# Optimization experiments

Hardware: AMD Instinct MI355X
Metric: run time of the kernel (lower is better)

Reference implementation:

```python
import jax, jax.numpy as jnp
import numpy as np

L_IN, L_ENC, B = 1024, 1024, 16
D_IN, D_ENC, D_EMB = 512, 512, 512


def setup_inputs() -> dict:
    key = jax.random.key(0)
    ks = jax.random.split(key, 9)
    s_in = 1.0 / np.sqrt(D_IN)
    s_emb = 1.0 / np.sqrt(D_EMB)
    s_enc = 1.0 / np.sqrt(D_ENC)
    return {
        "in_seq": jax.random.normal(ks[0], (L_IN, B, D_IN), jnp.float32),
        "enc_seq": jax.random.normal(ks[1], (L_ENC, B, D_ENC), jnp.float32),
        "prev_target_seq": jax.random.normal(ks[2], (L_IN, B, D_EMB), jnp.float32),
        # torch Linear weights: (out_features, in_features)
        "W_in2enc": jax.random.normal(ks[3], (D_ENC, D_IN), jnp.float32) * s_in,
        "b_in2enc": jnp.zeros((D_ENC,), jnp.float32),
        "W_lab2enc": jax.random.normal(ks[4], (D_ENC, D_EMB), jnp.float32) * s_emb,
        "b_lab2enc": jnp.zeros((D_ENC,), jnp.float32),
        "W_enc2in": jax.random.normal(ks[5], (D_IN, D_ENC), jnp.float32) * s_enc,
        "b_enc2in": jnp.zeros((D_IN,), jnp.float32),
    }


def reference(in_seq, enc_seq, prev_target_seq,
              W_in2enc, b_in2enc, W_lab2enc, b_lab2enc, W_enc2in, b_enc2in):
    # d_vals: (L_in, B, D_enc) = proj(in_seq) + proj(prev_target_seq)
    in_proj = jnp.einsum('lbi,ei->lbe', in_seq, W_in2enc) + b_in2enc
    tgt_proj = jnp.einsum('lbm,em->lbe', prev_target_seq, W_lab2enc) + b_lab2enc
    d_vals = in_proj + tgt_proj
    # raw attention scores: (L_in, L_enc, B) dot products over D_enc
    scores = jnp.einsum('lbe,mbe->lmb', d_vals, enc_seq)
    # sum-normalization (NOT softmax) over the encoder-length axis
    attn = scores / jnp.sum(scores, axis=1, keepdims=True)
    # weighted sum of encoder states: (L_in, B, D_enc)
    context = jnp.einsum('lmb,mbe->lbe', attn, enc_seq)
    # project back to input dim
    return jnp.einsum('lbe,ie->lbi', context, W_enc2in) + b_enc2in
```

## Files before the change

kernel.cpp:

```cpp
#include <hip/hip_runtime.h>
#include <cstdint>

static constexpr int LDR = 8192;

typedef uint16_t u16;
typedef __attribute__((ext_vector_type(8))) short short8;
typedef __attribute__((ext_vector_type(4))) float f32x4;
struct alignas(8) U16x4 { u16 x, y, z, w; };

__device__ __forceinline__ u16 f2bf(float f) {
    union { float f; unsigned u; } v; v.f = f;
    unsigned r = v.u + 0x7fffu + ((v.u >> 16) & 1u);
    return (u16)(r >> 16);
}

__device__ __forceinline__ short8 cvt8(const float4 a, const float4 b) {
    short8 r;
    r[0]=(short)f2bf(a.x); r[1]=(short)f2bf(a.y); r[2]=(short)f2bf(a.z); r[3]=(short)f2bf(a.w);
    r[4]=(short)f2bf(b.x); r[5]=(short)f2bf(b.y); r[6]=(short)f2bf(b.z); r[7]=(short)f2bf(b.w);
    return r;
}

__device__ __forceinline__ void gl_lds16(const u16* g, unsigned ldsaddr) {
    asm volatile("s_mov_b32 m0, %0\n\t"
                 "global_load_lds_dwordx4 %1, off"
                 :: "s"(__builtin_amdgcn_readfirstlane(ldsaddr)), "v"(g)
                 : "memory");
}

template<int MODE>
__device__ __forceinline__ void gemm_body(
    int bx, int by, int z,
    const u16* __restrict__ A, const u16* __restrict__ Bm,
    const float* __restrict__ b1v, const float* __restrict__ b2v,
    const float* __restrict__ b3v, const float* __restrict__ Sinv,
    u16* __restrict__ Cb, float* __restrict__ Cf)
{
    constexpr int K   = (MODE == 1 || MODE == 5) ? 1024 : 512;
    constexpr int BM  = (MODE == 5 || MODE == 6) ? 64 : 128;
    constexpr int NJ  = (BM == 128) ? 4 : 2;
    constexpr int NIA = BM / 64;
    constexpr int NIB = 2;
    constexpr int ASZ = BM * 64;
    constexpr int BSZ = 128 * 64;
    constexpr int LDA = (MODE == 1 || MODE == 5) ? 1024 : 512;
    constexpr int LDB = (MODE == 1 || MODE == 5) ? 1024 : 512;
    constexpr bool PRIO = (MODE == 5 || MODE == 6);

    extern __shared__ __align__(16) u16 lds[];

    const int row0 = by * BM;
    const int col0 = bx * 128;
    const int tid  = threadIdx.x;
    const int l    = tid & 63, w = tid >> 6;
    const int wm   = (BM == 128) ? (w >> 1) : 0;
    const int wn   = (BM == 128) ? (w & 1) : w;
    const int quad = l >> 4, l16 = l & 15;

    const u16* Ab = A;
    const u16* Bb = Bm;
    if constexpr (MODE == 5) { Ab = A + z*524288; Bb = Bm + z*524288; }
    if constexpr (MODE == 6) { Bb = Bm + z*262144; }
    if constexpr (MODE == 4) { Ab = A + z*524288; Bb = Bm + z*262144; }

    const int lr = l >> 2;
    const int loffu = ((l & 3) ^ (lr & 3)) * 8;
    const u16* gA[NIA];
    #pragma unroll
    for (int i = 0; i < NIA; ++i)
        gA[i] = Ab + (size_t)(row0 + i*64 + w*16 + lr) * LDA + loffu;
    const u16* gB[NIB];
    #pragma unroll
    for (int i = 0; i < NIB; ++i)
        gB[i] = Bb + (size_t)(col0 + i*64 + w*16 + lr) * LDB + loffu;

    const unsigned lbase = (unsigned)(size_t)&lds[0];

    auto stage = [&](int c) {
        #pragma unroll
        for (int i = 0; i < NIA; ++i) {
            gl_lds16(gA[i], lbase + c*ASZ + i*4096 + w*1024);
            gA[i] += 32;
        }
        #pragma unroll
        for (int i = 0; i < NIB; ++i) {
            gl_lds16(gB[i], lbase + 2*ASZ + c*BSZ + i*4096 + w*1024);
            gB[i] += 32;
        }
    };

    f32x4 acc[4][NJ] = {};
    const int swzr = (l16 & 3) << 3;
    const int arow = wm * 64;
    const int brow = wn * (BM == 128 ? 64 : 32);
    const int koff = (quad * 8) ^ swzr;

    stage(0);
    int cur = 0;
    for (int kb = 0; kb < K; kb += 32) {
        asm volatile("s_waitcnt vmcnt(0)" ::: "memory");
        __syncthreads();
        if (kb + 32 < K) stage(cur ^ 1);
        const int abase = cur * (ASZ/2);
        const int bbase = ASZ + cur * (BSZ/2);
        short8 af[4], bfr[NJ];
        #pragma unroll
        for (int i = 0; i < 4; ++i)
            af[i] = *(const short8*)&lds[abase + (arow + i*16 + l16)*32 + koff];
        #pragma unroll
        for (int j = 0; j < NJ; ++j)
            bfr[j] = *(const short8*)&lds[bbase + (brow + j*16 + l16)*32 + koff];
        if constexpr (PRIO) __builtin_amdgcn_s_setprio(1);
        #pragma unroll
        for (int i = 0; i < 4; ++i)
            #pragma unroll
            for (int j = 0; j < NJ; ++j)
                acc[i][j] = __builtin_amdgcn_mfma_f32_16x16x32_bf16(af[i], bfr[j], acc[i][j], 0, 0, 0);
        if constexpr (PRIO) __builtin_amdgcn_s_setprio(0);
        __syncthreads();
        cur ^= 1;
    }

    #pragma unroll
    for (int i = 0; i < 4; ++i) {
        const int grow = row0 + arow + i*16 + quad*4;
        #pragma unroll
        for (int j = 0; j < NJ; ++j) {
            const int gcol = col0 + brow + j*16 + l16;
            #pragma unroll
            for (int r = 0; r < 4; ++r) {
                float v = acc[i][j][r];
                const int R = grow + r;
                if constexpr (MODE == 1) {
                    v += b1v[gcol] + b2v[gcol];
                    Cb[((R & 15)*1024 + (R >> 4))*512 + gcol] = f2bf(v);
                } else if constexpr (MODE == 5 || MODE == 6) {
                    Cb[z*262144 + R*512 + gcol] = f2bf(v);
                } else {
                    const float s = Sinv[R*16 + z];
                    Cf[(R*16 + z)*512 + gcol] = v * s + b3v[gcol];
                }
            }
        }
    }
}

__device__ __forceinline__ void s_xt_body(
    int bid, const float* __restrict__ X, const float* __restrict__ T,
    const double* __restrict__ u, const double* __restrict__ cd,
    float* __restrict__ Sinv, u16* __restrict__ XT)
{
    const int wave = threadIdx.x >> 6, lane = threadIdx.x & 63;
    const int b = bid & 15, g = bid >> 4;
    const int e = lane * 8;
    double u1r[8], u2r[8];
    #pragma unroll
    for (int k = 0; k < 8; ++k) {
        u1r[k] = u[b*512 + e + k];
        u2r[k] = u[8192 + b*512 + e + k];
    }
    const double cb = cd[b];
    #pragma unroll 2
    for (int i = 0; i < 8; ++i) {
        const int j = g*32 + wave*8 + i;
        const int r = j*16 + b;
        float4 x0 = *(const float4*)&X[r*512 + e];
        float4 x1 = *(const float4*)&X[r*512 + e + 4];
        float4 t0 = *(const float4*)&T[r*512 + e];
        float4 t1 = *(const float4*)&T[r*512 + e + 4];
        double a = 0.0;
        a += (double)x0.x*u1r[0] + (double)x0.y*u1r[1] + (double)x0.z*u1r[2] + (double)x0.w*u1r[3];
        a += (double)x1.x*u1r[4] + (double)x1.y*u1r[5] + (double)x1.z*u1r[6] + (double)x1.w*u1r[7];
        a += (double)t0.x*u2r[0] + (double)t0.y*u2r[1] + (double)t0.z*u2r[2] + (double)t0.w*u2r[3];
        a += (double)t1.x*u2r[4] + (double)t1.y*u2r[5] + (double)t1.z*u2r[6] + (double)t1.w*u2r[7];
        *(short8*)&XT[r*1024 + e]       = cvt8(x0, x1);
        *(short8*)&XT[r*1024 + 512 + e] = cvt8(t0, t1);
        #pragma unroll
        for (int off = 32; off > 0; off >>= 1) a += __shfl_down(a, off, 64);
        if (lane == 0) Sinv[r] = (float)(1.0 / (a + cb));
    }
}

__global__ __launch_bounds__(256) void enct_wconv(
    const float* __restrict__ E, u16* __restrict__ EncT, double* __restrict__ part,
    const float* __restrict__ W1, const float* __restrict__ W2,
    const float* __restrict__ W3, u16* __restrict__ W12, u16* __restrict__ W3b)
{
    const int bid = blockIdx.x, t = threadIdx.x;
    if (bid >= 2048) {
        const int idx = (bid - 2048)*256 + t;
        if (idx < 65536) {
            const int r = idx >> 7, k8 = (idx & 127) * 8;
            const float* src = (k8 < 512) ? (W1 + r*512 + k8) : (W2 + r*512 + (k8 - 512));
            float4 a = *(const float4*)src;
            float4 b = *((const float4*)src + 1);
            *(short8*)&W12[r*1024 + k8] = cvt8(a, b);
        } else {
            const int i2 = idx - 65536;
            const int r = i2 >> 6, k8 = (i2 & 63) * 8;
            const float* src = W3 + r*512 + k8;
            float4 a = *(const float4*)src;
            float4 b = *((const float4*)src + 1);
            *(short8*)&W3b[r*512 + k8] = cvt8(a, b);
        }
        return;
    }
    __shared__ float tile[64][65];
    __shared__ double sred[256];
    const int ex = bid & 7;
    const int my = (bid >> 3) & 15;
    const int bb = bid >> 7;
    const int m0 = my * 64;
    const int e0 = ex * 64;
    const int tr = t >> 4;
    const int tc4 = (t & 15) * 4;
    #pragma unroll
    for (int it = 0; it < 4; ++it) {
        const int ml = tr + it*16;
        float4 v = *(const float4*)&E[(m0+ml)*LDR + bb*512 + e0 + tc4];
        *(float4*)&tile[ml][tc4] = v;
    }
    __syncthreads();
    #pragma unroll
    for (int it = 0; it < 4; ++it) {
        const int el = tr + it*16;
        U16x4 o;
        o.x = f2bf(tile[tc4+0][el]);
        o.y = f2bf(tile[tc4+1][el]);
        o.z = f2bf(tile[tc4+2][el]);
        o.w = f2bf(tile[tc4+3][el]);
        *(U16x4*)&EncT[bb*524288 + (e0+el)*1024 + m0 + tc4] = o;
    }
    const int el = t & 63, mq = t >> 6;
    double a = 0.0;
    #pragma unroll
    for (int j = 0; j < 16; ++j) a += (double)tile[mq*16 + j][el];
    sred[t] = a;
    __syncthreads();
    if (t < 64) {
        double s = sred[t] + sred[t+64] + sred[t+128] + sred[t+192];
        part[my*8192 + bb*512 + e0 + t] = s;
    }
}

__global__ __launch_bounds__(256) void g5_prep(
    const u16* __restrict__ EncT, u16* __restrict__ Gram,
    const float* __restrict__ W1, const float* __restrict__ W2,
    const float* __restrict__ b1, const float* __restrict__ b2,
    const double* __restrict__ part, double* __restrict__ u, double* __restrict__ cd)
{
    const int bid = blockIdx.x, tid = threadIdx.x;
    if (bid < 512) {
        gemm_body<5>(bid & 3, (bid >> 2) & 7, bid >> 5,
                     EncT, EncT, nullptr, nullptr, nullptr, nullptr, Gram, nullptr);
        return;
    }
    extern __shared__ __align__(16) u16 lds[];
    double* es_l = (double*)lds;
    double* red  = (double*)((char*)lds + 4096);
    const int blk = bid - 512;
    int b;
    if (blk < 64) b = (blk & 31) >> 1;
    else          b = blk - 64;
    for (int e = tid; e < 512; e += 256) {
        double s = 0.0;
        #pragma unroll
        for (int c = 0; c < 16; ++c) s += part[c*8192 + b*512 + e];
        es_l[e] = s;
    }
    __syncthreads();
    if (blk < 64) {
        const int which = blk >> 5;
        const int t = (blk & 31)*256 + tid;
        const int i = t & 511;
        const float* W = which ? W2 : W1;
        double a = 0.0;
        for (int e = 0; e < 512; ++e) a += (double)W[e*512 + i] * es_l[e];
        u[which*8192 + t] = a;
    } else {
        double a = 0.0;
        for (int e = tid; e < 512; e += 256) a += (double)(b1[e] + b2[e]) * es_l[e];
        red[tid] = a; __syncthreads();
        for (int s = 128; s > 0; s >>= 1) { if (tid < s) red[tid] += red[tid+s]; __syncthreads(); }
        if (tid == 0) cd[b] = red[0];
    }
}

__global__ __launch_bounds__(256) void g6_sxt(
    const u16* __restrict__ W3b, const u16* __restrict__ Gram, u16* __restrict__ HT,
    const float* __restrict__ X, const float* __restrict__ T,
    const double* __restrict__ u, const double* __restrict__ cd,
    float* __restrict__ Sinv, u16* __restrict__ XT)
{
    const int bid = blockIdx.x;
    const int idx = bid >> 1;
    if (bid & 1) {
        s_xt_body(idx, X, T, u, cd, Sinv, XT);
    } else {
        gemm_body<6>(idx & 3, (idx >> 2) & 7, idx >> 5,
                     W3b, Gram, nullptr, nullptr, nullptr, nullptr, HT, nullptr);
    }
}

__global__ __launch_bounds__(256) void gemm_m1(
    const u16* __restrict__ XT, const u16* __restrict__ W12,
    const float* __restrict__ b1, const float* __restrict__ b2,
    u16* __restrict__ dvals_g)
{
    const int bid = blockIdx.x;
    const int logical = (bid & 7)*64 + (bid >> 3);
    gemm_body<1>(logical & 3, logical >> 2, 0,
                 XT, W12, b1, b2, nullptr, nullptr, dvals_g, nullptr);
}

__global__ __launch_bounds__(256) void gemm_m4(
    const u16* __restrict__ dvals_g, const u16* __restrict__ HT,
    const float* __restrict__ b3, const float* __restrict__ Sinv,
    float* __restrict__ out)
{
    const int bid = blockIdx.x;
    const int logical = (bid & 7)*64 + (bid >> 3);
    gemm_body<4>(logical & 3, (logical >> 2) & 7, logical >> 5,
                 dvals_g, HT, nullptr, nullptr, b3, Sinv, nullptr, out);
}

extern "C" void kernel_launch(void* const* d_in, const int* in_sizes, int n_in,
                              void* d_out, int out_size, void* d_ws, size_t ws_size,
                              hipStream_t stream)
{
    const float* X   = (const float*)d_in[0];
    const float* Enc = (const float*)d_in[1];
    const float* T   = (const float*)d_in[2];
    const float* W1  = (const float*)d_in[3];
    const float* b1  = (const float*)d_in[4];
    const float* W2  = (const float*)d_in[5];
    const float* b2  = (const float*)d_in[6];
    const float* W3  = (const float*)d_in[7];
    const float* b3  = (const float*)d_in[8];
    float* out = (float*)d_out;

    char* w = (char*)d_ws;
    u16*    dvals_g  = (u16*)(w);
    u16*    EncT_bf  = (u16*)(w + 16777216);
    u16*    Gram_bf  = (u16*)(w + 33554432);
    u16*    HT_bf    = (u16*)(w + 41943040);
    u16*    W12      = (u16*)(w + 50331648);
    u16*    W3b      = (u16*)(w + 51380224);
    double* part     = (double*)(w + 51904512);
    double* u        = (double*)(w + 52953088);
    double* cd       = (double*)(w + 53084160);
    float*  Sinv     = (float*)(w + 53084288);
    u16*    XTb      = (u16*)d_out;

    dim3 blk(256);
    enct_wconv <<<dim3(2432), blk, 0,     stream>>>(Enc, EncT_bf, part, W1, W2, W3, W12, W3b);
    g5_prep    <<<dim3(592),  blk, 24576, stream>>>(EncT_bf, Gram_bf, W1, W2, b1, b2, part, u, cd);
    g6_sxt     <<<dim3(1024), blk, 24576, stream>>>(W3b, Gram_bf, HT_bf, X, T, u, cd, Sinv, XTb);
    gemm_m1    <<<dim3(512),  blk, 32768, stream>>>(XTb, W12, b1, b2, dvals_g);
    gemm_m4    <<<dim3(512),  blk, 32768, stream>>>(dvals_g, HT_bf, b3, Sinv, out);
}
```

Before: 241.9 us.

## Regroup GEMM stages across kernels and drop redundant per-iteration barrier

The small prep reduction becomes its own 80-block kernel. The Gram GEMM moves next to the S/XT computation, and the HT GEMM is co-launched with the dvals GEMM, so independent work shares launches and fills the device. The trailing __syncthreads in the double-buffered K loop is removed, since the barrier at the top of the next iteration already protects buffer reuse. The LDS XOR swizzle now keys on row bits 1–2 instead of 0–1 to change the bank-conflict pattern. Correctness relies on the new kernel order satisfying all data dependencies and on the write and read swizzles staying matched.

```diff
diff --git a/kernel.cpp b/kernel.cpp
--- a/kernel.cpp
+++ b/kernel.cpp
@@ -64,7 +64,7 @@
     if constexpr (MODE == 4) { Ab = A + z*524288; Bb = Bm + z*262144; }
 
     const int lr = l >> 2;
-    const int loffu = ((l & 3) ^ (lr & 3)) * 8;
+    const int loffu = ((l & 3) ^ ((lr >> 1) & 3)) * 8;
     const u16* gA[NIA];
     #pragma unroll
     for (int i = 0; i < NIA; ++i)
@@ -90,7 +90,7 @@
     };
 
     f32x4 acc[4][NJ] = {};
-    const int swzr = (l16 & 3) << 3;
+    const int swzr = ((l16 >> 1) & 3) << 3;
     const int arow = wm * 64;
     const int brow = wn * (BM == 128 ? 64 : 32);
     const int koff = (quad * 8) ^ swzr;
@@ -117,7 +117,6 @@
             for (int j = 0; j < NJ; ++j)
                 acc[i][j] = __builtin_amdgcn_mfma_f32_16x16x32_bf16(af[i], bfr[j], acc[i][j], 0, 0, 0);
         if constexpr (PRIO) __builtin_amdgcn_s_setprio(0);
-        __syncthreads();
         cur ^= 1;
     }
 
@@ -243,22 +242,14 @@
     }
 }
 
-__global__ __launch_bounds__(256) void g5_prep(
-    const u16* __restrict__ EncT, u16* __restrict__ Gram,
+__global__ __launch_bounds__(256) void prep80(
     const float* __restrict__ W1, const float* __restrict__ W2,
     const float* __restrict__ b1, const float* __restrict__ b2,
     const double* __restrict__ part, double* __restrict__ u, double* __restrict__ cd)
 {
-    const int bid = blockIdx.x, tid = threadIdx.x;
-    if (bid < 512) {
-        gemm_body<5>(bid & 3, (bid >> 2) & 7, bid >> 5,
-                     EncT, EncT, nullptr, nullptr, nullptr, nullptr, Gram, nullptr);
-        return;
-    }
-    extern __shared__ __align__(16) u16 lds[];
-    double* es_l = (double*)lds;
-    double* red  = (double*)((char*)lds + 4096);
-    const int blk = bid - 512;
+    const int blk = blockIdx.x, tid = threadIdx.x;
+    __shared__ double es_l[512];
+    __shared__ double red[256];
     int b;
     if (blk < 64) b = (blk & 31) >> 1;
     else          b = blk - 64;
@@ -286,31 +277,38 @@
     }
 }
 
-__global__ __launch_bounds__(256) void g6_sxt(
-    const u16* __restrict__ W3b, const u16* __restrict__ Gram, u16* __restrict__ HT,
+__global__ __launch_bounds__(256) void sxt_g5(
     const float* __restrict__ X, const float* __restrict__ T,
     const double* __restrict__ u, const double* __restrict__ cd,
-    float* __restrict__ Sinv, u16* __restrict__ XT)
+    float* __restrict__ Sinv, u16* __restrict__ XT,
+    const u16* __restrict__ EncT, u16* __restrict__ Gram)
 {
     const int bid = blockIdx.x;
     const int idx = bid >> 1;
     if (bid & 1) {
         s_xt_body(idx, X, T, u, cd, Sinv, XT);
     } else {
+        gemm_body<5>(idx & 3, (idx >> 2) & 7, idx >> 5,
+                     EncT, EncT, nullptr, nullptr, nullptr, nullptr, Gram, nullptr);
+    }
+}
+
+__global__ __launch_bounds__(256) void m1_g6(
+    const u16* __restrict__ XT, const u16* __restrict__ W12,
+    const float* __restrict__ b1, const float* __restrict__ b2,
+    u16* __restrict__ dvals_g,
+    const u16* __restrict__ W3b, const u16* __restrict__ Gram, u16* __restrict__ HT)
+{
+    const int bid = blockIdx.x;
+    const int idx = bid >> 1;
+    if ((bid & 1) == 0) {
+        const int logical = (idx & 7)*64 + (idx >> 3);
+        gemm_body<1>(logical & 3, logical >> 2, 0,
+                     XT, W12, b1, b2, nullptr, nullptr, dvals_g, nullptr);
+    } else {
         gemm_body<6>(idx & 3, (idx >> 2) & 7, idx >> 5,
                      W3b, Gram, nullptr, nullptr, nullptr, nullptr, HT, nullptr);
     }
-}
-
-__global__ __launch_bounds__(256) void gemm_m1(
-    const u16* __restrict__ XT, const u16* __restrict__ W12,
-    const float* __restrict__ b1, const float* __restrict__ b2,
-    u16* __restrict__ dvals_g)
-{
-    const int bid = blockIdx.x;
-    const int logical = (bid & 7)*64 + (bid >> 3);
-    gemm_body<1>(logical & 3, logical >> 2, 0,
-                 XT, W12, b1, b2, nullptr, nullptr, dvals_g, nullptr);
 }
 
 __global__ __launch_bounds__(256) void gemm_m4(
@@ -354,8 +352,8 @@
 
     dim3 blk(256);
     enct_wconv <<<dim3(2432), blk, 0,     stream>>>(Enc, EncT_bf, part, W1, W2, W3, W12, W3b);
-    g5_prep    <<<dim3(592),  blk, 24576, stream>>>(EncT_bf, Gram_bf, W1, W2, b1, b2, part, u, cd);
-    g6_sxt     <<<dim3(1024), blk, 24576, stream>>>(W3b, Gram_bf, HT_bf, X, T, u, cd, Sinv, XTb);
-    gemm_m1    <<<dim3(512),  blk, 32768, stream>>>(XTb, W12, b1, b2, dvals_g);
+    prep80     <<<dim3(80),   blk, 0,     stream>>>(W1, W2, b1, b2, part, u, cd);
+    sxt_g5     <<<dim3(1024), blk, 24576, stream>>>(X, T, u, cd, Sinv, XTb, EncT_bf, Gram_bf);
+    m1_g6      <<<dim3(1024), blk, 32768, stream>>>(XTb, W12, b1, b2, dvals_g, W3b, Gram_bf, HT_bf);
     gemm_m4    <<<dim3(512),  blk, 32768, stream>>>(dvals_g, HT_bf, b3, Sinv, out);
 }
```

Result: slower. 259.9 us (+7.4%).
